# Optimization experiments

Measured on AMD Instinct MI355X. Metric: run time of the kernel, lower is better.

The kernel has to match this reference:

```python
import jax, jax.numpy as jnp
import numpy as np

DIM = 768
HEADS = 12


def setup_inputs() -> dict:
    key = jax.random.key(0)
    ks = jax.random.split(key, 8)
    B, N, C = 4, 1024, DIM
    x = jax.random.normal(ks[0], (B, N, C), dtype=jnp.float32)
    mask = jax.random.normal(ks[1], (B, 1, N, N), dtype=jnp.float32)
    weight = jax.random.uniform(ks[2], (B, N), dtype=jnp.float32)
    s = 1.0 / np.sqrt(C)
    qkv_w = jax.random.normal(ks[3], (3 * C, C), dtype=jnp.float32) * s
    mu_w = jax.random.normal(ks[4], (C, C // 2), dtype=jnp.float32) * s
    mu_b = jnp.zeros((C,), dtype=jnp.float32)
    ls_w = jax.random.normal(ks[5], (C, C // 2), dtype=jnp.float32) * s
    ls_b = jnp.zeros((C,), dtype=jnp.float32)
    return {"x": x, "mask": mask, "weight": weight, "qkv_w": qkv_w,
            "mu_w": mu_w, "mu_b": mu_b, "ls_w": ls_w, "ls_b": ls_b}


def reference(x, mask, weight, qkv_w, mu_w, mu_b, ls_w, ls_b):
    B, N, C = x.shape
    H = HEADS
    Dh = C // H
    # NOTE: module uses head_dim = dim * num_heads for the scale (quirk, kept faithful)
    scale = (C * H) ** (-0.5)
    qkv = (x @ qkv_w.T).reshape(B, N, 3, H, Dh).transpose(2, 0, 3, 1, 4)  # [3,B,H,N,Dh]
    q, k, v = qkv[0], qkv[1], qkv[2]
    attn = jnp.einsum('bhnd,bhmd->bhnm', q, k) * scale + mask  # [B,H,N,N]
    attn = jax.nn.softmax(attn, axis=-1)
    # weight: [B,N] broadcast over heads and queries (key axis)
    w = weight[:, None, None, :] + 1e-10
    attn = attn * w
    attn = attn / attn.sum(axis=-1, keepdims=True)
    out = jnp.einsum('bhnm,bhmd->bhnd', attn, v)          # [B,H,N,Dh]
    out = out.transpose(0, 2, 1, 3).reshape(B, N, C)      # [B,N,C]
    mu_in = out[:, :, :C // 2]
    ls_in = out[:, :, C // 2:]
    mu = mu_in @ mu_w.T + mu_b
    logsigma = ls_in @ ls_w.T + ls_b
    return (mu, logsigma, attn)
```

## Files before the change

### kernel.cpp

```cpp
#include <hip/hip_runtime.h>
#include <hip/hip_bf16.h>

typedef __attribute__((ext_vector_type(8))) short short8;
typedef __attribute__((ext_vector_type(4))) float f32x4;
typedef __attribute__((ext_vector_type(4))) unsigned short u16x4;

#define NB 4
#define NN 1024
#define NC 768
#define NH 12
#define TC 2304

#define OFF_XB   0ul
#define OFF_WQ   6291456ul
#define OFF_WMU  (OFF_WQ + 3538944ul)
#define OFF_WLS  (OFF_WMU + 589824ul)
#define OFF_QKVB (OFF_WLS + 589824ul)
#define OFF_V3   (OFF_QKVB + 18874368ul)
#define OFF_OUTB (OFF_V3 + 6291456ul)

__device__ __forceinline__ unsigned short f2bf(float f) {
    unsigned int u = __float_as_uint(f);
    u = (u + 0x7FFFu + ((u >> 16) & 1u)) >> 16;
    return (unsigned short)u;
}

__device__ __forceinline__ void gload_lds16(const unsigned short* g, unsigned short* l) {
    __builtin_amdgcn_global_load_lds(
        (const __attribute__((address_space(1))) unsigned int*)g,
        (__attribute__((address_space(3))) unsigned int*)l, 16, 0, 0);
}

__device__ __forceinline__ void gload16(short8& dst, const unsigned short* p) {
    asm volatile("global_load_dwordx4 %0, %1, off" : "=v"(dst) : "v"(p));
}
__device__ __forceinline__ void gloadf4(f32x4& dst, const float* p) {
    asm volatile("global_load_dwordx4 %0, %1, off" : "=v"(dst) : "v"(p));
}
#define WAITV(N) do { asm volatile("s_waitcnt vmcnt(" #N ")" ::: "memory"); \
                      __builtin_amdgcn_sched_barrier(0); } while (0)
#define SBAR()   __builtin_amdgcn_sched_barrier(0)

__global__ void cast_all(const float* __restrict__ x, const float* __restrict__ qkv_w,
                         const float* __restrict__ mu_w, const float* __restrict__ ls_w,
                         unsigned short* __restrict__ dst) {
    int i = blockIdx.x * blockDim.x + threadIdx.x;
    const float* src; int off;
    if (i < 786432)            { src = x;     off = i; }
    else if (i < 1228800)      { src = qkv_w; off = i - 786432; }
    else if (i < 1302528)      { src = mu_w;  off = i - 1228800; }
    else                       { src = ls_w;  off = i - 1302528; }
    f32x4 v = ((const f32x4*)src)[off];
    u16x4 o;
#pragma unroll
    for (int j = 0; j < 4; ++j) o[j] = f2bf(v[j]);
    ((u16x4*)dst)[i] = o;
}

template <int EPI>
__device__ __forceinline__ void gemm_body(
    unsigned short* As, unsigned short* Bs,
    const unsigned short* __restrict__ A, const unsigned short* __restrict__ Bm,
    int K, int lda, int ldb, void* __restrict__ Cout, int ldc,
    const float* __restrict__ bias, int row0, int col0,
    unsigned short* __restrict__ v3)
{
    const int t = threadIdx.x;
    const int lane = t & 63;
    const int wv = t >> 6;
    const int wm = wv >> 1, wn = wv & 1;
    const int li = lane & 15;
    const int koff = (lane >> 4) * 8;

    f32x4 acc[4][4] = {};

    const int tr = t >> 2;
    const int tc = (t & 3) * 8;
    const unsigned short* ag = A + (size_t)(row0 + tr) * lda + tc;
    const unsigned short* bg = Bm + (size_t)(col0 + tr) * ldb + tc;

    for (int kt = 0; kt < K; kt += 32) {
        gload_lds16(ag,            As + t * 8);
        gload_lds16(ag + 64 * lda, As + 2048 + t * 8);
        gload_lds16(bg,            Bs + t * 8);
        gload_lds16(bg + 64 * ldb, Bs + 2048 + t * 8);
        ag += 32; bg += 32;
        __syncthreads();
        short8 af[4], bf[4];
#pragma unroll
        for (int m = 0; m < 4; ++m)
            af[m] = *(const short8*)&As[(wm * 64 + m * 16 + li) * 32 + koff];
#pragma unroll
        for (int n = 0; n < 4; ++n)
            bf[n] = *(const short8*)&Bs[(wn * 64 + n * 16 + li) * 32 + koff];
#pragma unroll
        for (int m = 0; m < 4; ++m)
#pragma unroll
            for (int n = 0; n < 4; ++n)
                acc[m][n] = __builtin_amdgcn_mfma_f32_16x16x32_bf16(af[m], bf[n], acc[m][n], 0, 0, 0);
        __syncthreads();
    }

#pragma unroll
    for (int m = 0; m < 4; ++m) {
        const int row = row0 + wm * 64 + m * 16 + (lane >> 4) * 4;
#pragma unroll
        for (int n = 0; n < 4; ++n) {
            const int col = col0 + wn * 64 + n * 16 + li;
#pragma unroll
            for (int r = 0; r < 4; ++r) {
                if (EPI == 1) {
                    ((float*)Cout)[(size_t)(row + r) * ldc + col] = acc[m][n][r] + bias[col];
                } else {
                    unsigned short bv = f2bf(acc[m][n][r]);
                    if (col0 >= 1536) {
                        const int rr = row + r;
                        const int b_ = rr >> 10, n_ = rr & 1023;
                        const int hd = col - 1536;
                        const int bh_ = b_ * NH + (hd >> 6);
                        const int d_ = hd & 63;
                        v3[(((size_t)bh_ * 32 + (n_ >> 5)) * 64 + d_) * 32 + (n_ & 31)] = bv;
                    } else {
                        ((unsigned short*)Cout)[(size_t)(row + r) * ldc + col] = bv;
                    }
                }
            }
        }
    }
}

__global__ __launch_bounds__(256, 2) void gemm_qkv(
    const unsigned short* __restrict__ A, const unsigned short* __restrict__ Bm,
    unsigned short* __restrict__ C, unsigned short* __restrict__ v3)
{
    __shared__ unsigned short As[128 * 32];
    __shared__ unsigned short Bs[128 * 32];
    const int bid = blockIdx.y * gridDim.x + blockIdx.x;
    const int nwg = gridDim.x * gridDim.y;
    const int swz = (bid & 7) * (nwg >> 3) + (bid >> 3);
    const int row0 = (swz / gridDim.x) * 128;
    const int col0 = (swz % gridDim.x) * 128;
    gemm_body<2>(As, Bs, A, Bm, NC, NC, NC, C, TC, nullptr, row0, col0, v3);
}

__global__ __launch_bounds__(256, 2) void gemm_heads(
    const unsigned short* __restrict__ outb,
    const unsigned short* __restrict__ wmu, const unsigned short* __restrict__ wls,
    const float* __restrict__ mu_b, const float* __restrict__ ls_b,
    float* __restrict__ out_mu, float* __restrict__ out_ls)
{
    __shared__ unsigned short As[128 * 32];
    __shared__ unsigned short Bs[128 * 32];
    const int bid = blockIdx.y * gridDim.x + blockIdx.x;
    const int nwg = gridDim.x * gridDim.y;
    const int swz = (bid & 7) * (nwg >> 3) + (bid >> 3);
    const int row0 = (swz / gridDim.x) * 128;
    const int col0 = (swz % gridDim.x) * 128;
    const int z = blockIdx.z;
    gemm_body<1>(As, Bs, outb + (z ? 384 : 0), z ? wls : wmu, 384, NC, 384,
                 z ? (void*)out_ls : (void*)out_mu, NC, z ? ls_b : mu_b, row0, col0, nullptr);
}

__global__ __launch_bounds__(512, 6) void attn_kernel(
    const unsigned short* __restrict__ qkvb, const unsigned short* __restrict__ v3,
    const float* __restrict__ mask, const float* __restrict__ weight,
    float* __restrict__ attn_out, unsigned short* __restrict__ outb)
{
    __shared__ __align__(16) char smem[33024];
    __shared__ f32x4 po[4][64];
    __shared__ float red_max[8][16];
    __shared__ float red_sum[8][16];

    const int t = threadIdx.x;
    const int lane = t & 63;
    const int wv = t >> 6;
    const int li = lane & 15;
    const int g = lane >> 4;
    const int koff = g * 8;
    const int bh = blockIdx.y;
    const int b = bh / NH, h = bh % NH;
    const int n0 = blockIdx.x * 16;

    unsigned short* sm = (unsigned short*)smem;

    const float* mrow = mask + (size_t)b * NN * NN + (size_t)(n0 + li) * NN + wv * 16 + g * 4;
    const unsigned short* kgbase = qkvb + (size_t)(b * NN) * TC + 768 + h * 64;

    const unsigned short* qp = qkvb + (size_t)(b * NN + n0 + li) * TC + h * 64 + koff;
    short8 qf0, qf1;
    gload16(qf0, qp);
    gload16(qf1, qp + 32);

    f32x4 acc[8];
    f32x4 mk[2];

#define KISSUE(c) do {                                                        \
        _Pragma("unroll")                                                     \
        for (int i_ = 0; i_ < 2; ++i_) {                                      \
            int m_ = wv * 16 + i_ * 8 + (lane >> 3);                          \
            int sl_ = (lane & 7) ^ (m_ & 7);                                  \
            const unsigned short* src_ = kgbase + (size_t)((c) * 128 + m_) * TC + sl_ * 8; \
            unsigned short* dst_ = sm + ((c) & 1) * 8192 + wv * 1024 + i_ * 512 + lane * 8; \
            gload_lds16(src_, dst_);                                          \
        }                                                                     \
        gloadf4(mk[(c) & 1], mrow + (c) * 128);                               \
    } while (0)

#define KSTEP(c) do {                                                         \
        const unsigned short* kbuf_ = sm + ((c) & 1) * 8192;                  \
        short8 kf0 = *(const short8*)&kbuf_[(wv * 16 + li) * 64 + ((g ^ (li & 7)) * 8)];       \
        short8 kf1 = *(const short8*)&kbuf_[(wv * 16 + li) * 64 + (((g + 4) ^ (li & 7)) * 8)]; \
        f32x4 ci = mk[(c) & 1] * 96.0f;                                       \
        ci = __builtin_amdgcn_mfma_f32_16x16x32_bf16(kf0, qf0, ci, 0, 0, 0);  \
        ci = __builtin_amdgcn_mfma_f32_16x16x32_bf16(kf1, qf1, ci, 0, 0, 0);  \
        acc[(c)] = ci;                                                        \
    } while (0)

    KISSUE(0); KISSUE(1);
    WAITV(3);  KSTEP(0); SBAR(); KISSUE(2);
    WAITV(3);  KSTEP(1); SBAR(); KISSUE(3);
    WAITV(3);  KSTEP(2); SBAR(); KISSUE(4);
    WAITV(3);  KSTEP(3); SBAR(); KISSUE(5);
    WAITV(3);  KSTEP(4); SBAR(); KISSUE(6);
    WAITV(3);  KSTEP(5); SBAR(); KISSUE(7);
    WAITV(3);  KSTEP(6);
    WAITV(0);  KSTEP(7);
#undef KISSUE
#undef KSTEP

    const float scale = 1.0f / 96.0f;
    float rmax = -1e30f;
#pragma unroll
    for (int cf = 0; cf < 8; ++cf) {
#pragma unroll
        for (int r = 0; r < 4; ++r) rmax = fmaxf(rmax, acc[cf][r]);
    }
    rmax = fmaxf(rmax, __shfl_xor(rmax, 16, 64));
    rmax = fmaxf(rmax, __shfl_xor(rmax, 32, 64));
    if (lane < 16) red_max[wv][lane] = rmax;
    __syncthreads();
    {
        float m01 = fmaxf(red_max[0][li], red_max[1][li]);
        float m23 = fmaxf(red_max[2][li], red_max[3][li]);
        float m45 = fmaxf(red_max[4][li], red_max[5][li]);
        float m67 = fmaxf(red_max[6][li], red_max[7][li]);
        rmax = fmaxf(fmaxf(m01, m23), fmaxf(m45, m67)) * scale;
    }

    unsigned short (*P)[1032] = (unsigned short(*)[1032])smem;
    const float* wbase = weight + b * NN + wv * 16 + g * 4;
    float rsum = 0.f;
#pragma unroll
    for (int cf = 0; cf < 8; ++cf) {
        f32x4 wcf = *(const f32x4*)(wbase + cf * 128);
        u16x4 pb;
#pragma unroll
        for (int r = 0; r < 4; ++r) {
            float p = __expf(acc[cf][r] * scale - rmax) * (wcf[r] + 1e-10f);
            acc[cf][r] = p;
            rsum += p;
            pb[r] = f2bf(p);
        }
        *(u16x4*)&P[li][cf * 128 + wv * 16 + g * 4] = pb;
    }
    rsum += __shfl_xor(rsum, 16, 64);
    rsum += __shfl_xor(rsum, 32, 64);
    if (lane < 16) red_sum[wv][lane] = rsum;
    __syncthreads();

    const float rinv = 1.0f / (red_sum[0][li] + red_sum[1][li] + red_sum[2][li]
                             + red_sum[3][li] + red_sum[4][li] + red_sum[5][li]
                             + red_sum[6][li] + red_sum[7][li]);
    float* arow = attn_out + (size_t)bh * NN * NN + (size_t)(n0 + li) * NN + wv * 16 + g * 4;
#pragma unroll
    for (int cf = 0; cf < 8; ++cf) {
        f32x4 a4;
#pragma unroll
        for (int r = 0; r < 4; ++r) a4[r] = acc[cf][r] * rinv;
        __builtin_nontemporal_store(a4, (f32x4*)(arow + cf * 128));
    }

    const int kh = wv >> 2, p4 = wv & 3;
    f32x4 o = {};
    const unsigned short* v3s = v3 + (size_t)bh * 65536 + (size_t)(kh * 16) * 2048
                              + p4 * 512 + li * 32 + g * 8;
    short8 vA[4], vB[4];
#define VISSUE(c, vb2) do {                                                   \
        _Pragma("unroll")                                                     \
        for (int j2 = 0; j2 < 4; ++j2) gload16(vb2[j2], v3s + ((c) * 4 + j2) * 2048); \
    } while (0)
#define VCOMP(c, vb2) do {                                                    \
        __builtin_amdgcn_s_setprio(1);                                        \
        _Pragma("unroll")                                                     \
        for (int j2 = 0; j2 < 4; ++j2) {                                      \
            const int kt = kh * 16 + (c) * 4 + j2;                            \
            short8 pa = *(const short8*)&P[li][kt * 32 + koff];               \
            o = __builtin_amdgcn_mfma_f32_16x16x32_bf16(pa, vb2[j2], o, 0, 0, 0); \
        }                                                                     \
        __builtin_amdgcn_s_setprio(0);                                        \
    } while (0)
    VISSUE(0, vA);
    VISSUE(1, vB);
    WAITV(4);  VCOMP(0, vA); SBAR(); VISSUE(2, vA);
    WAITV(4);  VCOMP(1, vB); SBAR(); VISSUE(3, vB);
    WAITV(4);  VCOMP(2, vA);
    WAITV(0);  VCOMP(3, vB);
#undef VISSUE
#undef VCOMP

    if (kh == 1) po[p4][lane] = o;
    __syncthreads();
    if (kh == 0) {
        f32x4 oo = po[p4][lane];
        const int dcol = h * 64 + p4 * 16 + li;
#pragma unroll
        for (int r = 0; r < 4; ++r) {
            const int row = g * 4 + r;
            const float rs = red_sum[0][row] + red_sum[1][row] + red_sum[2][row]
                           + red_sum[3][row] + red_sum[4][row] + red_sum[5][row]
                           + red_sum[6][row] + red_sum[7][row];
            outb[(size_t)(b * NN + n0 + row) * NC + dcol] = f2bf((o[r] + oo[r]) / rs);
        }
    }
}

extern "C" void kernel_launch(void* const* d_in, const int* in_sizes, int n_in,
                              void* d_out, int out_size, void* d_ws, size_t ws_size,
                              hipStream_t stream) {
    const float* x      = (const float*)d_in[0];
    const float* mask   = (const float*)d_in[1];
    const float* weight = (const float*)d_in[2];
    const float* qkv_w  = (const float*)d_in[3];
    const float* mu_w   = (const float*)d_in[4];
    const float* mu_b   = (const float*)d_in[5];
    const float* ls_w   = (const float*)d_in[6];
    const float* ls_b   = (const float*)d_in[7];

    char* ws = (char*)d_ws;
    unsigned short* xb   = (unsigned short*)(ws + OFF_XB);
    unsigned short* wq   = (unsigned short*)(ws + OFF_WQ);
    unsigned short* wmu  = (unsigned short*)(ws + OFF_WMU);
    unsigned short* wls  = (unsigned short*)(ws + OFF_WLS);
    unsigned short* qkvb = (unsigned short*)(ws + OFF_QKVB);
    unsigned short* v3   = (unsigned short*)(ws + OFF_V3);
    unsigned short* outb = (unsigned short*)(ws + OFF_OUTB);

    float* out_mu   = (float*)d_out;
    float* out_ls   = out_mu + 3145728;
    float* out_attn = out_mu + 6291456;

    cast_all<<<5376, 256, 0, stream>>>(x, qkv_w, mu_w, ls_w, xb);

    gemm_qkv<<<dim3(TC / 128, 4096 / 128), 256, 0, stream>>>(xb, wq, qkvb, v3);

    attn_kernel<<<dim3(NN / 16, NB * NH), 512, 0, stream>>>(
        qkvb, v3, mask, weight, out_attn, outb);

    gemm_heads<<<dim3(NC / 128, 4096 / 128, 2), 256, 0, stream>>>(
        outb, wmu, wls, mu_b, ls_b, out_mu, out_ls);
}
```

Before: 148.6 us.

## Move V transpose into separate LDS pack kernel and prefetch weights early

Removes the scattered 2-byte V stores from the QKV GEMM epilogue. The GEMM now writes all of qkv row-major, and a new pack_v kernel transposes V through shared memory into the blocked v3 layout with vector stores. Separately, the attention kernel issues the per-key weight loads before the max reduction and waits on them in two halves, so their latency overlaps the reduction. The cost is an extra kernel launch plus an extra read and write of V, in exchange for coalesced stores.

```diff
diff --git a/kernel.cpp b/kernel.cpp
--- a/kernel.cpp
+++ b/kernel.cpp
@@ -62,8 +62,7 @@
     unsigned short* As, unsigned short* Bs,
     const unsigned short* __restrict__ A, const unsigned short* __restrict__ Bm,
     int K, int lda, int ldb, void* __restrict__ Cout, int ldc,
-    const float* __restrict__ bias, int row0, int col0,
-    unsigned short* __restrict__ v3)
+    const float* __restrict__ bias, int row0, int col0)
 {
     const int t = threadIdx.x;
     const int lane = t & 63;
@@ -109,20 +108,10 @@
             const int col = col0 + wn * 64 + n * 16 + li;
 #pragma unroll
             for (int r = 0; r < 4; ++r) {
-                if (EPI == 1) {
+                if (EPI == 0) {
+                    ((unsigned short*)Cout)[(size_t)(row + r) * ldc + col] = f2bf(acc[m][n][r]);
+                } else {
                     ((float*)Cout)[(size_t)(row + r) * ldc + col] = acc[m][n][r] + bias[col];
-                } else {
-                    unsigned short bv = f2bf(acc[m][n][r]);
-                    if (col0 >= 1536) {
-                        const int rr = row + r;
-                        const int b_ = rr >> 10, n_ = rr & 1023;
-                        const int hd = col - 1536;
-                        const int bh_ = b_ * NH + (hd >> 6);
-                        const int d_ = hd & 63;
-                        v3[(((size_t)bh_ * 32 + (n_ >> 5)) * 64 + d_) * 32 + (n_ & 31)] = bv;
-                    } else {
-                        ((unsigned short*)Cout)[(size_t)(row + r) * ldc + col] = bv;
-                    }
                 }
             }
         }
@@ -131,7 +120,7 @@
 
 __global__ __launch_bounds__(256, 2) void gemm_qkv(
     const unsigned short* __restrict__ A, const unsigned short* __restrict__ Bm,
-    unsigned short* __restrict__ C, unsigned short* __restrict__ v3)
+    unsigned short* __restrict__ C)
 {
     __shared__ unsigned short As[128 * 32];
     __shared__ unsigned short Bs[128 * 32];
@@ -140,7 +129,7 @@
     const int swz = (bid & 7) * (nwg >> 3) + (bid >> 3);
     const int row0 = (swz / gridDim.x) * 128;
     const int col0 = (swz % gridDim.x) * 128;
-    gemm_body<2>(As, Bs, A, Bm, NC, NC, NC, C, TC, nullptr, row0, col0, v3);
+    gemm_body<0>(As, Bs, A, Bm, NC, NC, NC, C, TC, nullptr, row0, col0);
 }
 
 __global__ __launch_bounds__(256, 2) void gemm_heads(
@@ -158,7 +147,39 @@
     const int col0 = (swz % gridDim.x) * 128;
     const int z = blockIdx.z;
     gemm_body<1>(As, Bs, outb + (z ? 384 : 0), z ? wls : wmu, 384, NC, 384,
-                 z ? (void*)out_ls : (void*)out_mu, NC, z ? ls_b : mu_b, row0, col0, nullptr);
+                 z ? (void*)out_ls : (void*)out_mu, NC, z ? ls_b : mu_b, row0, col0);
+}
+
+__global__ __launch_bounds__(256, 4) void pack_v(
+    const unsigned short* __restrict__ qkvb, unsigned short* __restrict__ v3)
+{
+    __shared__ unsigned short tile[64][65];
+    const int t = threadIdx.x;
+    const int bh = blockIdx.y;
+    const int b = bh / NH, h = bh % NH;
+    const int m0 = blockIdx.x * 64;
+#pragma unroll
+    for (int i = 0; i < 2; ++i) {
+        int lin = i * 256 + t;
+        int mr = lin >> 3;
+        int dr = (lin & 7) * 8;
+        short8 v = *(const short8*)(qkvb + (size_t)(b * NN + m0 + mr) * TC + 1536 + h * 64 + dr);
+#pragma unroll
+        for (int j = 0; j < 8; ++j) tile[mr][dr + j] = (unsigned short)v[j];
+    }
+    __syncthreads();
+#pragma unroll
+    for (int i = 0; i < 2; ++i) {
+        int lin = i * 256 + t;
+        int dw = lin >> 3;
+        int mw = (lin & 7) * 8;
+        short8 v;
+#pragma unroll
+        for (int j = 0; j < 8; ++j) v[j] = (short)tile[mw + j][dw];
+        int kt = (m0 + mw) >> 5;
+        int mm = mw & 31;
+        *(short8*)(v3 + ((size_t)(bh * 32 + kt) * 64 + dw) * 32 + mm) = v;
+    }
 }
 
 __global__ __launch_bounds__(512, 6) void attn_kernel(
@@ -228,6 +249,11 @@
 #undef KISSUE
 #undef KSTEP
 
+    const float* wbase = weight + b * NN + wv * 16 + g * 4;
+    f32x4 wreg[8];
+#pragma unroll
+    for (int cf = 0; cf < 8; ++cf) gloadf4(wreg[cf], wbase + cf * 128);
+
     const float scale = 1.0f / 96.0f;
     float rmax = -1e30f;
 #pragma unroll
@@ -248,15 +274,27 @@
     }
 
     unsigned short (*P)[1032] = (unsigned short(*)[1032])smem;
-    const float* wbase = weight + b * NN + wv * 16 + g * 4;
     float rsum = 0.f;
-#pragma unroll
-    for (int cf = 0; cf < 8; ++cf) {
-        f32x4 wcf = *(const f32x4*)(wbase + cf * 128);
+    WAITV(4);
+#pragma unroll
+    for (int cf = 0; cf < 4; ++cf) {
         u16x4 pb;
 #pragma unroll
         for (int r = 0; r < 4; ++r) {
-            float p = __expf(acc[cf][r] * scale - rmax) * (wcf[r] + 1e-10f);
+            float p = __expf(acc[cf][r] * scale - rmax) * (wreg[cf][r] + 1e-10f);
+            acc[cf][r] = p;
+            rsum += p;
+            pb[r] = f2bf(p);
+        }
+        *(u16x4*)&P[li][cf * 128 + wv * 16 + g * 4] = pb;
+    }
+    WAITV(0);
+#pragma unroll
+    for (int cf = 4; cf < 8; ++cf) {
+        u16x4 pb;
+#pragma unroll
+        for (int r = 0; r < 4; ++r) {
+            float p = __expf(acc[cf][r] * scale - rmax) * (wreg[cf][r] + 1e-10f);
             acc[cf][r] = p;
             rsum += p;
             pb[r] = f2bf(p);
@@ -351,7 +389,9 @@
 
     cast_all<<<5376, 256, 0, stream>>>(x, qkv_w, mu_w, ls_w, xb);
 
-    gemm_qkv<<<dim3(TC / 128, 4096 / 128), 256, 0, stream>>>(xb, wq, qkvb, v3);
+    gemm_qkv<<<dim3(TC / 128, 4096 / 128), 256, 0, stream>>>(xb, wq, qkvb);
+
+    pack_v<<<dim3(NN / 64, NB * NH), 256, 0, stream>>>(qkvb, v3);
 
     attn_kernel<<<dim3(NN / 16, NB * NH), 512, 0, stream>>>(
         qkvb, v3, mask, weight, out_attn, outb);
```

Result: faster. 143.6 us (-3.4%).
